# Kernel optimization log

Measured on AMD Instinct MI355X. Metric: run time of the kernel, lower is better.

The kernel has to match this reference:

```python
import jax, jax.numpy as jnp
import numpy as np

N_NODES = 50000
N_EDGES = 300000
D = 256
N_RELS = 500


def setup_inputs() -> dict:
    key = jax.random.key(0)
    ks = jax.random.split(key, 12)
    s = 1.0 / np.sqrt(D)  # keep activations O(1) through the dense transforms
    return {
        "h": jax.random.normal(ks[0], (N_NODES, D), dtype=jnp.float32),
        "prev_h": jax.random.normal(ks[1], (N_NODES, D), dtype=jnp.float32),
        "emb_rel": jax.random.normal(ks[2], (N_RELS, D), dtype=jnp.float32),
        "norm": jax.random.uniform(ks[3], (N_NODES, 1), dtype=jnp.float32),
        "weight_neighbor": jax.random.normal(ks[4], (D, D), dtype=jnp.float32) * s,
        "loop_weight": jax.random.normal(ks[5], (D, D), dtype=jnp.float32) * s,
        "evolve_loop_weight": jax.random.normal(ks[6], (D, D), dtype=jnp.float32) * s,
        "skip_connect_weight": jax.random.normal(ks[7], (D, D), dtype=jnp.float32) * s,
        "skip_connect_bias": jnp.zeros((D,), dtype=jnp.float32),
        "src": jax.random.randint(ks[8], (N_EDGES,), 0, N_NODES),
        "dst": jax.random.randint(ks[9], (N_EDGES,), 0, N_NODES),
        "etype": jax.random.randint(ks[10], (N_EDGES,), 0, N_RELS),
    }


def reference(h, prev_h, emb_rel, norm, weight_neighbor, loop_weight,
              evolve_loop_weight, skip_connect_weight, skip_connect_bias,
              src, dst, etype):
    n_nodes = h.shape[0]
    # msg_func: per-edge gather of src features + relation embedding, dense transform
    msg = (h[src] + emb_rel[etype]) @ weight_neighbor          # [E, D]
    # fn.sum: segment-sum messages into destination nodes
    agg = jax.ops.segment_sum(msg, dst, num_segments=n_nodes)  # [N, D]
    # apply_func: multiply by per-node norm
    agg = agg * norm
    # self-loop: loop_weight where in_degree > 0, evolve_loop_weight otherwise
    in_deg = jax.ops.segment_sum(jnp.ones_like(dst), dst, num_segments=n_nodes)
    has_in = (in_deg > 0)[:, None]
    loop_message = jnp.where(has_in, h @ loop_weight, h @ evolve_loop_weight)
    # skip connection gate
    skip_weight = jax.nn.sigmoid(prev_h @ skip_connect_weight + skip_connect_bias)
    node_repr = skip_weight * (agg + loop_message) + (1.0 - skip_weight) * prev_h
    return jax.nn.relu(node_repr)
```

## Files before the change

### kernel.cpp

```cpp
#include <hip/hip_runtime.h>
#include <cstdint>
#include <cstddef>

#define N_NODES 50000
#define N_EDGES 300000
#define DIM     256
#define KTOT    768
#define N_RELS  500

#define SCAN_BLK  256
#define SCAN_NBLK ((N_NODES + SCAN_BLK - 1) / SCAN_BLK)

#define CONV_ELEMS ((N_NODES + N_RELS) * DIM)
#define CONV_BLKS  ((CONV_ELEMS / 8 + 255) / 256)
#define HIST_BLKS  ((N_EDGES + 255) / 256)

typedef unsigned short u16;
typedef __attribute__((ext_vector_type(8))) short short8v;
typedef __attribute__((ext_vector_type(4))) float float4v;

static __device__ __forceinline__ u16 f2bf(float f) {
    union { float f; unsigned u; } v; v.f = f;
    unsigned u = v.u;
    unsigned r = u + 0x7FFFu + ((u >> 16) & 1u);
    return (u16)(r >> 16);
}
static __device__ __forceinline__ float bf2f(u16 b) {
    union { unsigned u; float f; } v; v.u = ((unsigned)b) << 16; return v.f;
}

static __device__ __forceinline__ void gld16(const void* g, u16* l) {
    __builtin_amdgcn_global_load_lds(
        (const __attribute__((address_space(1))) unsigned int*)g,
        (__attribute__((address_space(3))) unsigned int*)l,
        16, 0, 0);
}

__global__ void prep_kernel(const float* __restrict__ h, const float* __restrict__ emb,
                            const float* __restrict__ Wn, const float* __restrict__ Wl,
                            const float* __restrict__ Wsc, const int* __restrict__ dstv,
                            u16* __restrict__ Xh, u16* __restrict__ embb,
                            u16* __restrict__ Wt, int* __restrict__ deg) {
    int b = blockIdx.x;
    if (b < CONV_BLKS) {
        int i = b * 256 + threadIdx.x;
        int e0 = i * 8;
        if (e0 >= CONV_ELEMS) return;
        const float* s; u16* d;
        if (e0 < N_NODES * DIM) { s = h + e0; d = Xh + e0; }
        else { int o = e0 - N_NODES * DIM; s = emb + o; d = embb + o; }
        float4 a = *(const float4*)(s);
        float4 c2 = *(const float4*)(s + 4);
        u16 o8[8] = { f2bf(a.x), f2bf(a.y), f2bf(a.z), f2bf(a.w),
                      f2bf(c2.x), f2bf(c2.y), f2bf(c2.z), f2bf(c2.w) };
        *(uint4*)d = *(const uint4*)o8;
    } else if (b < CONV_BLKS + KTOT) {
        int k = b - CONV_BLKS;
        int dd = threadIdx.x;
        const float* W = (k < 256) ? Wn : ((k < 512) ? Wl : Wsc);
        Wt[(size_t)dd * KTOT + k] = f2bf(W[(k & 255) * DIM + dd]);
    } else {
        int e = (b - CONV_BLKS - KTOT) * 256 + threadIdx.x;
        if (e < N_EDGES) atomicAdd(&deg[dstv[e]], 1);
    }
}

__global__ void scanA_kernel(const int* __restrict__ deg, int* __restrict__ excl_local,
                             int* __restrict__ block_sum) {
    __shared__ int sdata[SCAN_BLK];
    int t = threadIdx.x, i = blockIdx.x * SCAN_BLK + t;
    int v = (i < N_NODES) ? deg[i] : 0;
    sdata[t] = v;
    __syncthreads();
    for (int off = 1; off < SCAN_BLK; off <<= 1) {
        int u = (t >= off) ? sdata[t - off] : 0;
        __syncthreads();
        sdata[t] += u;
        __syncthreads();
    }
    if (i < N_NODES) excl_local[i] = sdata[t] - v;
    if (t == SCAN_BLK - 1) block_sum[blockIdx.x] = sdata[t];
}

__global__ void scanB_kernel(const int* __restrict__ block_sum, int* __restrict__ block_base,
                             int* __restrict__ offsets) {
    __shared__ int sdata[SCAN_NBLK];
    int t = threadIdx.x;
    int v = (t < SCAN_NBLK) ? block_sum[t] : 0;
    if (t < SCAN_NBLK) sdata[t] = v;
    __syncthreads();
    for (int off = 1; off < SCAN_NBLK; off <<= 1) {
        int u = (t >= off && t < SCAN_NBLK) ? sdata[t - off] : 0;
        __syncthreads();
        if (t < SCAN_NBLK) sdata[t] += u;
        __syncthreads();
    }
    if (t < SCAN_NBLK) block_base[t] = sdata[t] - v;
    if (t == SCAN_NBLK - 1) offsets[N_NODES] = sdata[t];
}

__global__ void scanC_kernel(const int* __restrict__ excl_local, const int* __restrict__ block_base,
                             int* __restrict__ offsets, int* __restrict__ cursor) {
    int i = blockIdx.x * SCAN_BLK + threadIdx.x;
    if (i < N_NODES) {
        int e = block_base[blockIdx.x] + excl_local[i];
        offsets[i] = e; cursor[i] = e;
    }
}

__global__ void scatter_kernel(const int* __restrict__ src, const int* __restrict__ dstv,
                               const int* __restrict__ et, int* __restrict__ cursor,
                               unsigned* __restrict__ esee) {
    int e = blockIdx.x * 256 + threadIdx.x;
    if (e >= N_EDGES) return;
    int d = dstv[e];
    int pos = atomicAdd(&cursor[d], 1);
    esee[pos] = (unsigned)src[e] * N_RELS + (unsigned)et[e];
}

__global__ void agg_kernel(const u16* __restrict__ Xh, const u16* __restrict__ embb,
                           const float* __restrict__ norm, const int* __restrict__ offsets,
                           const unsigned* __restrict__ esee, const float* __restrict__ prev_h,
                           u16* __restrict__ Xa, u16* __restrict__ Xp,
                           int* __restrict__ wl_count, int* __restrict__ wl) {
    int wave = (blockIdx.x * 256 + threadIdx.x) >> 6;
    int lane = threadIdx.x & 63;
    if (wave >= N_NODES) return;
    int n = wave;
    int s0 = offsets[n], s1 = offsets[n + 1];
    int c4 = lane * 4;
    float4 pv = *(const float4*)(prev_h + (size_t)n * DIM + c4);
    float4 acc = make_float4(0.f, 0.f, 0.f, 0.f);
    int e = s0;
    for (; e + 3 < s1; e += 4) {
        unsigned v0 = esee[e], v1 = esee[e + 1], v2 = esee[e + 2], v3 = esee[e + 3];
        unsigned sa = v0 / N_RELS, ta = v0 - sa * N_RELS;
        unsigned sb = v1 / N_RELS, tb = v1 - sb * N_RELS;
        unsigned sc = v2 / N_RELS, tc = v2 - sc * N_RELS;
        unsigned sd = v3 / N_RELS, td = v3 - sd * N_RELS;
        ushort4 ha = *(const ushort4*)(Xh + (size_t)sa * DIM + c4);
        ushort4 ea = *(const ushort4*)(embb + (size_t)ta * DIM + c4);
        ushort4 hb = *(const ushort4*)(Xh + (size_t)sb * DIM + c4);
        ushort4 eb = *(const ushort4*)(embb + (size_t)tb * DIM + c4);
        ushort4 hc = *(const ushort4*)(Xh + (size_t)sc * DIM + c4);
        ushort4 ec = *(const ushort4*)(embb + (size_t)tc * DIM + c4);
        ushort4 hd = *(const ushort4*)(Xh + (size_t)sd * DIM + c4);
        ushort4 ed = *(const ushort4*)(embb + (size_t)td * DIM + c4);
        acc.x += (bf2f(ha.x) + bf2f(ea.x)) + (bf2f(hb.x) + bf2f(eb.x))
               + (bf2f(hc.x) + bf2f(ec.x)) + (bf2f(hd.x) + bf2f(ed.x));
        acc.y += (bf2f(ha.y) + bf2f(ea.y)) + (bf2f(hb.y) + bf2f(eb.y))
               + (bf2f(hc.y) + bf2f(ec.y)) + (bf2f(hd.y) + bf2f(ed.y));
        acc.z += (bf2f(ha.z) + bf2f(ea.z)) + (bf2f(hb.z) + bf2f(eb.z))
               + (bf2f(hc.z) + bf2f(ec.z)) + (bf2f(hd.z) + bf2f(ed.z));
        acc.w += (bf2f(ha.w) + bf2f(ea.w)) + (bf2f(hb.w) + bf2f(eb.w))
               + (bf2f(hc.w) + bf2f(ec.w)) + (bf2f(hd.w) + bf2f(ed.w));
    }
    for (; e < s1; e++) {
        unsigned v = esee[e];
        unsigned s = v / N_RELS;
        unsigned t = v - s * N_RELS;
        ushort4 hv = *(const ushort4*)(Xh + (size_t)s * DIM + c4);
        ushort4 ev = *(const ushort4*)(embb + (size_t)t * DIM + c4);
        acc.x += bf2f(hv.x) + bf2f(ev.x);
        acc.y += bf2f(hv.y) + bf2f(ev.y);
        acc.z += bf2f(hv.z) + bf2f(ev.z);
        acc.w += bf2f(hv.w) + bf2f(ev.w);
    }
    float nr = norm[n];
    u16 o[4] = { f2bf(acc.x * nr), f2bf(acc.y * nr), f2bf(acc.z * nr), f2bf(acc.w * nr) };
    *(ushort4*)(Xa + (size_t)n * DIM + c4) = *(const ushort4*)o;
    u16 p4[4] = { f2bf(pv.x), f2bf(pv.y), f2bf(pv.z), f2bf(pv.w) };
    *(ushort4*)(Xp + (size_t)n * DIM + c4) = *(const ushort4*)p4;
    if (lane == 0 && s1 == s0) { int idx = atomicAdd(wl_count, 1); wl[idx] = n; }
}

__launch_bounds__(512, 4)
__global__ void gemm_kernel(const u16* __restrict__ Xa, const u16* __restrict__ Xh,
                            const u16* __restrict__ Xp, const u16* __restrict__ Wt,
                            const float* __restrict__ prev_h, const float* __restrict__ bias,
                            float* __restrict__ out) {
    __shared__ __align__(16) u16 lds[40960];
    int tid  = threadIdx.x;
    int wave = tid >> 6, lane = tid & 63, q = lane >> 4, m16 = lane & 15;
    int wm = wave >> 2;
    int wnn = (wave & 3) * 64;
    int m0 = blockIdx.x * 64;
    int lr = lane >> 3, lc8 = lane & 7;
    int sc8 = (lc8 ^ lr) << 3;

    int arow = wave * 8 + lr;
    int ga = (m0 + arow < N_NODES) ? (m0 + arow) : (N_NODES - 1);
    const u16* sAa = Xa + (size_t)ga * DIM + sc8;
    const u16* sAh = Xh + (size_t)ga * DIM + sc8;
    const u16* sAp = Xp + (size_t)ga * DIM + sc8;
    const u16* sB = Wt + (size_t)(wave * 32 + lr) * KTOT + sc8;

    float4v acc1[2][4], acc2[2][4];
#pragma unroll
    for (int i = 0; i < 2; i++)
#pragma unroll
        for (int j = 0; j < 4; j++) { acc1[i][j] = (float4v)0.f; acc2[i][j] = (float4v)0.f; }

    auto stage = [&](int kt, int buf) {
#pragma unroll
        for (int j = 0; j < 4; j++)
            gld16(sB + (size_t)j * 8 * KTOT + kt * 64,
                  &lds[8192 + buf * 16384 + wave * 2048 + j * 512]);
        const u16* base = (kt < 4) ? sAa : ((kt < 8) ? sAh : sAp);
        gld16(base + (kt & 3) * 64, &lds[buf * 4096 + wave * 512]);
    };

    stage(0, 0);
    stage(1, 1);

    int sw = (m16 & 7) << 3;

#pragma unroll
    for (int kt = 0; kt < 12; kt++) {
        int buf = kt & 1;
        if (kt < 11) asm volatile("s_waitcnt vmcnt(5)" ::: "memory");
        else         asm volatile("s_waitcnt vmcnt(0)" ::: "memory");
        __builtin_amdgcn_sched_barrier(0);
        __builtin_amdgcn_s_barrier();
        __builtin_amdgcn_sched_barrier(0);

#pragma unroll
        for (int kk = 0; kk < 2; kk++) {
            int ck = (kk * 32 + q * 8) ^ sw;
            short8v af[2], bfr[4];
#pragma unroll
            for (int mi = 0; mi < 2; mi++)
                af[mi] = *(const short8v*)(&lds[buf * 4096 + (wm * 32 + mi * 16 + m16) * 64 + ck]);
#pragma unroll
            for (int ni = 0; ni < 4; ni++)
                bfr[ni] = *(const short8v*)(&lds[8192 + buf * 16384 + (wnn + ni * 16 + m16) * 64 + ck]);
            if (kt < 8) {
#pragma unroll
                for (int mi = 0; mi < 2; mi++)
#pragma unroll
                    for (int ni = 0; ni < 4; ni++)
                        acc1[mi][ni] = __builtin_amdgcn_mfma_f32_16x16x32_bf16(
                            af[mi], bfr[ni], acc1[mi][ni], 0, 0, 0);
            } else {
#pragma unroll
                for (int mi = 0; mi < 2; mi++)
#pragma unroll
                    for (int ni = 0; ni < 4; ni++)
                        acc2[mi][ni] = __builtin_amdgcn_mfma_f32_16x16x32_bf16(
                            af[mi], bfr[ni], acc2[mi][ni], 0, 0, 0);
            }
        }

        __builtin_amdgcn_sched_barrier(0);
        __builtin_amdgcn_s_barrier();
        __builtin_amdgcn_sched_barrier(0);
        if (kt + 2 < 12) stage(kt + 2, buf);
    }

#pragma unroll
    for (int mi = 0; mi < 2; mi++) {
#pragma unroll
        for (int ni = 0; ni < 4; ni++) {
            int d = wnn + ni * 16 + m16;
            float b = bias[d];
#pragma unroll
            for (int r = 0; r < 4; r++) {
                int node = m0 + wm * 32 + mi * 16 + q * 4 + r;
                if (node < N_NODES) {
                    float S  = acc2[mi][ni][r] + b;
                    float sg = 1.f / (1.f + __expf(-S));
                    float ph = prev_h[(size_t)node * DIM + d];
                    float v  = sg * acc1[mi][ni][r] + (1.f - sg) * ph;
                    out[(size_t)node * DIM + d] = fmaxf(v, 0.f);
                }
            }
        }
    }
}

__global__ void fixup_kernel(const float* __restrict__ h, const float* __restrict__ prev_h,
                             const float* __restrict__ We, const float* __restrict__ Wsc,
                             const float* __restrict__ bias, const int* __restrict__ wl_count,
                             const int* __restrict__ wl, float* __restrict__ out) {
    __shared__ float ph[DIM], hh[DIM];
    int d = threadIdx.x;
    int cnt = *wl_count;
    for (int i = blockIdx.x; i < cnt; i += gridDim.x) {
        int n = wl[i];
        ph[d] = prev_h[(size_t)n * DIM + d];
        hh[d] = h[(size_t)n * DIM + d];
        __syncthreads();
        float s = 0.f, l = 0.f;
        for (int k = 0; k < DIM; k++) {
            s += ph[k] * Wsc[k * DIM + d];
            l += hh[k] * We[k * DIM + d];
        }
        float sg = 1.f / (1.f + __expf(-(s + bias[d])));
        float v = sg * l + (1.f - sg) * ph[d];
        out[(size_t)n * DIM + d] = fmaxf(v, 0.f);
        __syncthreads();
    }
}

extern "C" void kernel_launch(void* const* d_in, const int* in_sizes, int n_in,
                              void* d_out, int out_size, void* d_ws, size_t ws_size,
                              hipStream_t stream) {
    const float* h      = (const float*)d_in[0];
    const float* prev_h = (const float*)d_in[1];
    const float* emb    = (const float*)d_in[2];
    const float* norm   = (const float*)d_in[3];
    const float* Wn     = (const float*)d_in[4];
    const float* Wl     = (const float*)d_in[5];
    const float* We     = (const float*)d_in[6];
    const float* Wsc    = (const float*)d_in[7];
    const float* bias   = (const float*)d_in[8];
    const int*   src    = (const int*)d_in[9];
    const int*   dstv   = (const int*)d_in[10];
    const int*   et     = (const int*)d_in[11];
    float* out = (float*)d_out;

    char* ws = (char*)d_ws;
    size_t off = 0;
    auto alloc = [&](size_t bytes) -> char* {
        char* p = ws + off; off += (bytes + 255) & ~(size_t)255; return p;
    };
    u16* Xa      = (u16*)alloc((size_t)N_NODES * DIM * 2);
    u16* Xh      = (u16*)alloc((size_t)N_NODES * DIM * 2);
    u16* Xp      = (u16*)alloc((size_t)N_NODES * DIM * 2);
    u16* embb    = (u16*)alloc((size_t)N_RELS * DIM * 2);
    u16* Wt      = (u16*)alloc((size_t)DIM * KTOT * 2);
    int* deg     = (int*)alloc((size_t)N_NODES * 4);
    int* wlcnt   = (int*)alloc(16);
    int* wl      = (int*)alloc((size_t)N_NODES * 4);
    int* offsets = (int*)alloc((size_t)(N_NODES + 1) * 4);
    int* cursor  = (int*)alloc((size_t)N_NODES * 4);
    unsigned* esee = (unsigned*)alloc((size_t)N_EDGES * 4);
    int* excl    = (int*)alloc((size_t)N_NODES * 4);
    int* bsum    = (int*)alloc((size_t)SCAN_NBLK * 4);
    int* bbase   = (int*)alloc((size_t)SCAN_NBLK * 4);

    hipMemsetAsync(deg, 0, (size_t)N_NODES * 4, stream);
    hipMemsetAsync(wlcnt, 0, 4, stream);

    prep_kernel<<<CONV_BLKS + KTOT + HIST_BLKS, 256, 0, stream>>>(
        h, emb, Wn, Wl, Wsc, dstv, Xh, embb, Wt, deg);
    scanA_kernel<<<SCAN_NBLK, SCAN_BLK, 0, stream>>>(deg, excl, bsum);
    scanB_kernel<<<1, SCAN_BLK, 0, stream>>>(bsum, bbase, offsets);
    scanC_kernel<<<SCAN_NBLK, SCAN_BLK, 0, stream>>>(excl, bbase, offsets, cursor);
    scatter_kernel<<<(N_EDGES + 255) / 256, 256, 0, stream>>>(src, dstv, et, cursor, esee);
    agg_kernel<<<(N_NODES + 3) / 4, 256, 0, stream>>>(Xh, embb, norm, offsets, esee, prev_h,
                                                      Xa, Xp, wlcnt, wl);
    gemm_kernel<<<(N_NODES + 63) / 64, 512, 0, stream>>>(Xa, Xh, Xp, Wt, prev_h, bias, out);
    fixup_kernel<<<256, 256, 0, stream>>>(h, prev_h, We, Wsc, bias, wlcnt, wl, out);
}
```

Baseline: 316.9 us.

## Tile weight transpose, single-kernel scan, and half-wave-per-node aggregation

The weight transpose now goes through an LDS tile in 48 blocks, so reads and writes are coalesced instead of each of 768 blocks doing strided writes. The three-kernel degree scan becomes one 1024-thread kernel, which removes two launches and the intermediate buffers. The aggregation kernel assigns a 32-lane half-wave to each node and loads 16 bytes per lane, giving wider gathers and more nodes in flight. The single-block scan is serial across its chunks, and the gather loop in each lane now holds more registers.

Measured after the change: 422.8 us. +33.4%, slower.

```diff
diff --git a/kernel.cpp b/kernel.cpp
--- a/kernel.cpp
+++ b/kernel.cpp
@@ -8,11 +8,9 @@
 #define KTOT    768
 #define N_RELS  500
 
-#define SCAN_BLK  256
-#define SCAN_NBLK ((N_NODES + SCAN_BLK - 1) / SCAN_BLK)
-
 #define CONV_ELEMS ((N_NODES + N_RELS) * DIM)
 #define CONV_BLKS  ((CONV_ELEMS / 8 + 255) / 256)
+#define WT_BLKS    48
 #define HIST_BLKS  ((N_EDGES + 255) / 256)
 
 typedef unsigned short u16;
@@ -36,11 +34,22 @@
         16, 0, 0);
 }
 
+static __device__ __forceinline__ void acc8(float* a, uint4 hv, uint4 ev) {
+    const unsigned* hw = (const unsigned*)&hv;
+    const unsigned* ew = (const unsigned*)&ev;
+#pragma unroll
+    for (int j = 0; j < 4; j++) {
+        a[2*j]   += bf2f((u16)(hw[j] & 0xffffu)) + bf2f((u16)(ew[j] & 0xffffu));
+        a[2*j+1] += bf2f((u16)(hw[j] >> 16))     + bf2f((u16)(ew[j] >> 16));
+    }
+}
+
 __global__ void prep_kernel(const float* __restrict__ h, const float* __restrict__ emb,
                             const float* __restrict__ Wn, const float* __restrict__ Wl,
                             const float* __restrict__ Wsc, const int* __restrict__ dstv,
                             u16* __restrict__ Xh, u16* __restrict__ embb,
                             u16* __restrict__ Wt, int* __restrict__ deg) {
+    __shared__ float T[64][65];
     int b = blockIdx.x;
     if (b < CONV_BLKS) {
         int i = b * 256 + threadIdx.x;
@@ -54,58 +63,59 @@
         u16 o8[8] = { f2bf(a.x), f2bf(a.y), f2bf(a.z), f2bf(a.w),
                       f2bf(c2.x), f2bf(c2.y), f2bf(c2.z), f2bf(c2.w) };
         *(uint4*)d = *(const uint4*)o8;
-    } else if (b < CONV_BLKS + KTOT) {
-        int k = b - CONV_BLKS;
-        int dd = threadIdx.x;
-        const float* W = (k < 256) ? Wn : ((k < 512) ? Wl : Wsc);
-        Wt[(size_t)dd * KTOT + k] = f2bf(W[(k & 255) * DIM + dd]);
+    } else if (b < CONV_BLKS + WT_BLKS) {
+        int tb  = b - CONV_BLKS;
+        int mat = tb >> 4;
+        int kb  = (tb & 15) >> 2;
+        int db  = tb & 3;
+        const float* W = (mat == 0) ? Wn : ((mat == 1) ? Wl : Wsc);
+        int c  = threadIdx.x & 63;
+        int rq = threadIdx.x >> 6;
+#pragma unroll
+        for (int p = 0; p < 16; p++) {
+            int kk = rq + p * 4;
+            T[kk][c] = W[(kb * 64 + kk) * DIM + db * 64 + c];
+        }
+        __syncthreads();
+#pragma unroll
+        for (int p = 0; p < 16; p++) {
+            int dd = rq + p * 4;
+            Wt[(size_t)(db * 64 + dd) * KTOT + mat * 256 + kb * 64 + c] = f2bf(T[c][dd]);
+        }
     } else {
-        int e = (b - CONV_BLKS - KTOT) * 256 + threadIdx.x;
+        int e = (b - CONV_BLKS - WT_BLKS) * 256 + threadIdx.x;
         if (e < N_EDGES) atomicAdd(&deg[dstv[e]], 1);
     }
 }
 
-__global__ void scanA_kernel(const int* __restrict__ deg, int* __restrict__ excl_local,
-                             int* __restrict__ block_sum) {
-    __shared__ int sdata[SCAN_BLK];
-    int t = threadIdx.x, i = blockIdx.x * SCAN_BLK + t;
-    int v = (i < N_NODES) ? deg[i] : 0;
-    sdata[t] = v;
+__global__ void scan_kernel(const int* __restrict__ deg, int* __restrict__ offsets,
+                            int* __restrict__ cursor) {
+    __shared__ int part[1024];
+    const int CH = (N_NODES + 1023) / 1024;
+    int t = threadIdx.x;
+    int base = t * CH;
+    int s = 0;
+    for (int i = 0; i < CH; i++) {
+        int idx = base + i;
+        if (idx < N_NODES) s += deg[idx];
+    }
+    part[t] = s;
     __syncthreads();
-    for (int off = 1; off < SCAN_BLK; off <<= 1) {
-        int u = (t >= off) ? sdata[t - off] : 0;
-        __syncthreads();
-        sdata[t] += u;
-        __syncthreads();
-    }
-    if (i < N_NODES) excl_local[i] = sdata[t] - v;
-    if (t == SCAN_BLK - 1) block_sum[blockIdx.x] = sdata[t];
-}
-
-__global__ void scanB_kernel(const int* __restrict__ block_sum, int* __restrict__ block_base,
-                             int* __restrict__ offsets) {
-    __shared__ int sdata[SCAN_NBLK];
-    int t = threadIdx.x;
-    int v = (t < SCAN_NBLK) ? block_sum[t] : 0;
-    if (t < SCAN_NBLK) sdata[t] = v;
-    __syncthreads();
-    for (int off = 1; off < SCAN_NBLK; off <<= 1) {
-        int u = (t >= off && t < SCAN_NBLK) ? sdata[t - off] : 0;
-        __syncthreads();
-        if (t < SCAN_NBLK) sdata[t] += u;
-        __syncthreads();
-    }
-    if (t < SCAN_NBLK) block_base[t] = sdata[t] - v;
-    if (t == SCAN_NBLK - 1) offsets[N_NODES] = sdata[t];
-}
-
-__global__ void scanC_kernel(const int* __restrict__ excl_local, const int* __restrict__ block_base,
-                             int* __restrict__ offsets, int* __restrict__ cursor) {
-    int i = blockIdx.x * SCAN_BLK + threadIdx.x;
-    if (i < N_NODES) {
-        int e = block_base[blockIdx.x] + excl_local[i];
-        offsets[i] = e; cursor[i] = e;
-    }
+    for (int off = 1; off < 1024; off <<= 1) {
+        int u = (t >= off) ? part[t - off] : 0;
+        __syncthreads();
+        part[t] += u;
+        __syncthreads();
+    }
+    int run = part[t] - s;
+    for (int i = 0; i < CH; i++) {
+        int idx = base + i;
+        if (idx < N_NODES) {
+            offsets[idx] = run; cursor[idx] = run;
+            run += deg[idx];
+        }
+    }
+    if (t == 1023) offsets[N_NODES] = part[1023];
 }
 
 __global__ void scatter_kernel(const int* __restrict__ src, const int* __restrict__ dstv,
@@ -124,13 +134,15 @@
                            u16* __restrict__ Xa, u16* __restrict__ Xp,
                            int* __restrict__ wl_count, int* __restrict__ wl) {
     int wave = (blockIdx.x * 256 + threadIdx.x) >> 6;
-    int lane = threadIdx.x & 63;
-    if (wave >= N_NODES) return;
-    int n = wave;
+    int half = (threadIdx.x >> 5) & 1;
+    int lane32 = threadIdx.x & 31;
+    int n = wave * 2 + half;
+    if (n >= N_NODES) return;
     int s0 = offsets[n], s1 = offsets[n + 1];
-    int c4 = lane * 4;
-    float4 pv = *(const float4*)(prev_h + (size_t)n * DIM + c4);
-    float4 acc = make_float4(0.f, 0.f, 0.f, 0.f);
+    int c8 = lane32 * 8;
+    float4 pa = *(const float4*)(prev_h + (size_t)n * DIM + c8);
+    float4 pb = *(const float4*)(prev_h + (size_t)n * DIM + c8 + 4);
+    float acc[8] = {0.f, 0.f, 0.f, 0.f, 0.f, 0.f, 0.f, 0.f};
     int e = s0;
     for (; e + 3 < s1; e += 4) {
         unsigned v0 = esee[e], v1 = esee[e + 1], v2 = esee[e + 2], v3 = esee[e + 3];
@@ -138,40 +150,33 @@
         unsigned sb = v1 / N_RELS, tb = v1 - sb * N_RELS;
         unsigned sc = v2 / N_RELS, tc = v2 - sc * N_RELS;
         unsigned sd = v3 / N_RELS, td = v3 - sd * N_RELS;
-        ushort4 ha = *(const ushort4*)(Xh + (size_t)sa * DIM + c4);
-        ushort4 ea = *(const ushort4*)(embb + (size_t)ta * DIM + c4);
-        ushort4 hb = *(const ushort4*)(Xh + (size_t)sb * DIM + c4);
-        ushort4 eb = *(const ushort4*)(embb + (size_t)tb * DIM + c4);
-        ushort4 hc = *(const ushort4*)(Xh + (size_t)sc * DIM + c4);
-        ushort4 ec = *(const ushort4*)(embb + (size_t)tc * DIM + c4);
-        ushort4 hd = *(const ushort4*)(Xh + (size_t)sd * DIM + c4);
-        ushort4 ed = *(const ushort4*)(embb + (size_t)td * DIM + c4);
-        acc.x += (bf2f(ha.x) + bf2f(ea.x)) + (bf2f(hb.x) + bf2f(eb.x))
-               + (bf2f(hc.x) + bf2f(ec.x)) + (bf2f(hd.x) + bf2f(ed.x));
-        acc.y += (bf2f(ha.y) + bf2f(ea.y)) + (bf2f(hb.y) + bf2f(eb.y))
-               + (bf2f(hc.y) + bf2f(ec.y)) + (bf2f(hd.y) + bf2f(ed.y));
-        acc.z += (bf2f(ha.z) + bf2f(ea.z)) + (bf2f(hb.z) + bf2f(eb.z))
-               + (bf2f(hc.z) + bf2f(ec.z)) + (bf2f(hd.z) + bf2f(ed.z));
-        acc.w += (bf2f(ha.w) + bf2f(ea.w)) + (bf2f(hb.w) + bf2f(eb.w))
-               + (bf2f(hc.w) + bf2f(ec.w)) + (bf2f(hd.w) + bf2f(ed.w));
+        uint4 ha = *(const uint4*)(Xh + (size_t)sa * DIM + c8);
+        uint4 ea = *(const uint4*)(embb + (size_t)ta * DIM + c8);
+        uint4 hb = *(const uint4*)(Xh + (size_t)sb * DIM + c8);
+        uint4 eb = *(const uint4*)(embb + (size_t)tb * DIM + c8);
+        uint4 hc = *(const uint4*)(Xh + (size_t)sc * DIM + c8);
+        uint4 ec = *(const uint4*)(embb + (size_t)tc * DIM + c8);
+        uint4 hd = *(const uint4*)(Xh + (size_t)sd * DIM + c8);
+        uint4 ed = *(const uint4*)(embb + (size_t)td * DIM + c8);
+        acc8(acc, ha, ea); acc8(acc, hb, eb); acc8(acc, hc, ec); acc8(acc, hd, ed);
     }
     for (; e < s1; e++) {
         unsigned v = esee[e];
         unsigned s = v / N_RELS;
         unsigned t = v - s * N_RELS;
-        ushort4 hv = *(const ushort4*)(Xh + (size_t)s * DIM + c4);
-        ushort4 ev = *(const ushort4*)(embb + (size_t)t * DIM + c4);
-        acc.x += bf2f(hv.x) + bf2f(ev.x);
-        acc.y += bf2f(hv.y) + bf2f(ev.y);
-        acc.z += bf2f(hv.z) + bf2f(ev.z);
-        acc.w += bf2f(hv.w) + bf2f(ev.w);
+        uint4 hv = *(const uint4*)(Xh + (size_t)s * DIM + c8);
+        uint4 ev = *(const uint4*)(embb + (size_t)t * DIM + c8);
+        acc8(acc, hv, ev);
     }
     float nr = norm[n];
-    u16 o[4] = { f2bf(acc.x * nr), f2bf(acc.y * nr), f2bf(acc.z * nr), f2bf(acc.w * nr) };
-    *(ushort4*)(Xa + (size_t)n * DIM + c4) = *(const ushort4*)o;
-    u16 p4[4] = { f2bf(pv.x), f2bf(pv.y), f2bf(pv.z), f2bf(pv.w) };
-    *(ushort4*)(Xp + (size_t)n * DIM + c4) = *(const ushort4*)p4;
-    if (lane == 0 && s1 == s0) { int idx = atomicAdd(wl_count, 1); wl[idx] = n; }
+    u16 o[8];
+#pragma unroll
+    for (int j = 0; j < 8; j++) o[j] = f2bf(acc[j] * nr);
+    *(uint4*)(Xa + (size_t)n * DIM + c8) = *(const uint4*)o;
+    u16 p8[8] = { f2bf(pa.x), f2bf(pa.y), f2bf(pa.z), f2bf(pa.w),
+                  f2bf(pb.x), f2bf(pb.y), f2bf(pb.z), f2bf(pb.w) };
+    *(uint4*)(Xp + (size_t)n * DIM + c8) = *(const uint4*)p8;
+    if (lane32 == 0 && s1 == s0) { int idx = atomicAdd(wl_count, 1); wl[idx] = n; }
 }
 
 __launch_bounds__(512, 4)
@@ -335,21 +340,16 @@
     int* offsets = (int*)alloc((size_t)(N_NODES + 1) * 4);
     int* cursor  = (int*)alloc((size_t)N_NODES * 4);
     unsigned* esee = (unsigned*)alloc((size_t)N_EDGES * 4);
-    int* excl    = (int*)alloc((size_t)N_NODES * 4);
-    int* bsum    = (int*)alloc((size_t)SCAN_NBLK * 4);
-    int* bbase   = (int*)alloc((size_t)SCAN_NBLK * 4);
 
     hipMemsetAsync(deg, 0, (size_t)N_NODES * 4, stream);
     hipMemsetAsync(wlcnt, 0, 4, stream);
 
-    prep_kernel<<<CONV_BLKS + KTOT + HIST_BLKS, 256, 0, stream>>>(
+    prep_kernel<<<CONV_BLKS + WT_BLKS + HIST_BLKS, 256, 0, stream>>>(
         h, emb, Wn, Wl, Wsc, dstv, Xh, embb, Wt, deg);
-    scanA_kernel<<<SCAN_NBLK, SCAN_BLK, 0, stream>>>(deg, excl, bsum);
-    scanB_kernel<<<1, SCAN_BLK, 0, stream>>>(bsum, bbase, offsets);
-    scanC_kernel<<<SCAN_NBLK, SCAN_BLK, 0, stream>>>(excl, bbase, offsets, cursor);
+    scan_kernel<<<1, 1024, 0, stream>>>(deg, offsets, cursor);
     scatter_kernel<<<(N_EDGES + 255) / 256, 256, 0, stream>>>(src, dstv, et, cursor, esee);
-    agg_kernel<<<(N_NODES + 3) / 4, 256, 0, stream>>>(Xh, embb, norm, offsets, esee, prev_h,
-                                                      Xa, Xp, wlcnt, wl);
+    agg_kernel<<<(N_NODES / 2 + 3) / 4, 256, 0, stream>>>(Xh, embb, norm, offsets, esee, prev_h,
+                                                          Xa, Xp, wlcnt, wl);
     gemm_kernel<<<(N_NODES + 63) / 64, 512, 0, stream>>>(Xa, Xh, Xp, Wt, prev_h, bias, out);
     fixup_kernel<<<256, 256, 0, stream>>>(h, prev_h, We, Wsc, bias, wlcnt, wl, out);
 }
```
